# Kernel optimization log

Hardware: AMD Instinct MI355X
Metric: run time of the kernel (lower is better)

The kernel has to match this reference:

```python
import jax, jax.numpy as jnp
import numpy as np

N_NODES = 100000
N_EDGES = 3200000


def _gcn_layer(x, W, b, src, dst, n):
    # DGL GraphConv, norm='both': D_out^{-1/2} A^T D_in^{-1/2} style normalization.
    ones = jnp.ones((src.shape[0],), dtype=x.dtype)
    deg_out = jnp.clip(jax.ops.segment_sum(ones, src, num_segments=n), 1.0)  # out-degree of src
    deg_in = jnp.clip(jax.ops.segment_sum(ones, dst, num_segments=n), 1.0)   # in-degree of dst
    # pre-normalize and project first (in_feats >= out_feats => cheaper messages)
    h = (x * jax.lax.rsqrt(deg_out)[:, None]) @ W            # [N, out]
    agg = jax.ops.segment_sum(h[src], dst, num_segments=n)   # gather + scatter-add over edges
    return agg * jax.lax.rsqrt(deg_in)[:, None] + b


def setup_inputs() -> dict:
    key = jax.random.key(0)
    k1, k2, k3, k4, k5 = jax.random.split(key, 5)
    in_f, h_f, n_cls = 256, 128, 40
    x = jax.random.normal(k1, (N_NODES, in_f), dtype=jnp.float32)
    W1 = jax.random.normal(k2, (in_f, h_f), dtype=jnp.float32) * (1.0 / np.sqrt(in_f))
    b1 = jnp.zeros((h_f,), dtype=jnp.float32)
    W2 = jax.random.normal(k3, (h_f, n_cls), dtype=jnp.float32) * (1.0 / np.sqrt(h_f))
    b2 = jnp.zeros((n_cls,), dtype=jnp.float32)
    src = jax.random.randint(k4, (N_EDGES,), 0, N_NODES, dtype=jnp.int32)
    dst = jax.random.randint(k5, (N_EDGES,), 0, N_NODES, dtype=jnp.int32)
    return {"x": x, "W1": W1, "b1": b1, "W2": W2, "b2": b2, "src": src, "dst": dst}


def reference(x, W1, b1, W2, b2, src, dst):
    n = x.shape[0]
    h = _gcn_layer(x, W1, b1, src, dst, n)
    h = jax.nn.relu(h)
    return _gcn_layer(h, W2, b2, src, dst, n)  # [N, num_classes] logits
```

## Files before the change

### kernel.cpp

```cpp
#include <hip/hip_runtime.h>

#define IN_F 256
#define HID  128
#define NCLS 40
#define NBKT 256
#define BKTSH 9
#define CH 16384
#define CAP 18432

typedef __attribute__((ext_vector_type(8))) short bf16x8;
typedef __attribute__((ext_vector_type(4))) float f32x4;

static __device__ __forceinline__ unsigned short f2bf(float f) {
    unsigned u = __builtin_bit_cast(unsigned, f);
    u += 0x7fffu + ((u >> 16) & 1u);
    return (unsigned short)(u >> 16);
}
static __device__ __forceinline__ float bf2f(unsigned short b) {
    return __builtin_bit_cast(float, ((unsigned)b) << 16);
}

__global__ void initcur_kernel(int* __restrict__ curD, int* __restrict__ curS) {
    int t = threadIdx.x;
    curD[t] = t * CAP;
    curS[t] = t * CAP;
}

__global__ __launch_bounds__(256) void binBoth_kernel(
    const int* __restrict__ src, const int* __restrict__ dst,
    int* __restrict__ curD, int* __restrict__ curS,
    int* __restrict__ bin, unsigned short* __restrict__ bin2, int E) {
    __shared__ int cntD[NBKT], ofsD[NBKT];
    __shared__ int cntS[NBKT], ofsS[NBKT];
    const int tx = threadIdx.x;
    const int be = blockIdx.x * CH;
    const int ee = min(be + CH, E);
    cntD[tx] = 0; cntS[tx] = 0;
    __syncthreads();
    for (int i = be + tx; i < ee; i += 256) {
        atomicAdd(&cntD[dst[i] >> BKTSH], 1);
        atomicAdd(&cntS[src[i] >> BKTSH], 1);
    }
    __syncthreads();
    int c = cntD[tx];
    ofsD[tx] = c ? atomicAdd(&curD[tx], c) : 0;
    cntD[tx] = 0;
    c = cntS[tx];
    ofsS[tx] = c ? atomicAdd(&curS[tx], c) : 0;
    cntS[tx] = 0;
    __syncthreads();
    for (int i = be + tx; i < ee; i += 256) {
        int d = dst[i], s = src[i];
        int b = d >> BKTSH;
        int l = atomicAdd(&cntD[b], 1);
        bin[ofsD[b] + l] = ((d & 511) << 17) | s;
        int b2 = s >> BKTSH;
        int l2 = atomicAdd(&cntS[b2], 1);
        bin2[ofsS[b2] + l2] = (unsigned short)(s & 511);
    }
}

__global__ __launch_bounds__(256) void passB_kernel(
    const int* __restrict__ curD_final, const int* __restrict__ bin,
    int* __restrict__ csr_src, int* __restrict__ row_ptr, int* __restrict__ row_end,
    float* __restrict__ rs_in, int N) {
    __shared__ int cnt[512];
    __shared__ int cur[512];
    __shared__ int part[256];
    const int b = blockIdx.x;
    const int base = b * CAP, end = curD_final[b];
    const int tx = threadIdx.x;
    cnt[tx] = 0; cnt[tx + 256] = 0;
    __syncthreads();
    for (int i = base + tx; i < end; i += 256)
        atomicAdd(&cnt[bin[i] >> 17], 1);
    __syncthreads();
    int a0 = cnt[2 * tx], a1 = cnt[2 * tx + 1];
    part[tx] = a0 + a1;
    __syncthreads();
    for (int off = 1; off < 256; off <<= 1) {
        int v = (tx >= off) ? part[tx - off] : 0;
        __syncthreads();
        part[tx] += v;
        __syncthreads();
    }
    int excl = part[tx] - (a0 + a1);
    cur[2 * tx] = excl;
    cur[2 * tx + 1] = excl + a0;
    int idx = (b << BKTSH) + 2 * tx;
    row_ptr[idx]     = base + excl;
    row_end[idx]     = base + excl + a0;
    row_ptr[idx + 1] = base + excl + a0;
    row_end[idx + 1] = base + excl + a0 + a1;
    if (idx < N)     rs_in[idx]     = rsqrtf((float)max(a0, 1));
    if (idx + 1 < N) rs_in[idx + 1] = rsqrtf((float)max(a1, 1));
    __syncthreads();
    for (int i = base + tx; i < end; i += 256) {
        int v = bin[i];
        int nl = v >> 17;
        int p = atomicAdd(&cur[nl], 1);
        csr_src[base + p] = v & 0x1FFFF;
    }
}

__global__ __launch_bounds__(256) void passBs_kernel(
    const int* __restrict__ curS_final, const unsigned short* __restrict__ bin2,
    float* __restrict__ rs_out, int N) {
    __shared__ int cnt[512];
    const int b = blockIdx.x;
    const int base = b * CAP, end = curS_final[b];
    const int tx = threadIdx.x;
    cnt[tx] = 0; cnt[tx + 256] = 0;
    __syncthreads();
    for (int i = base + tx; i < end; i += 256)
        atomicAdd(&cnt[bin2[i]], 1);
    __syncthreads();
    int idx = (b << BKTSH) + tx;
    if (idx < N)       rs_out[idx]       = rsqrtf((float)max(cnt[tx], 1));
    if (idx + 256 < N) rs_out[idx + 256] = rsqrtf((float)max(cnt[tx + 256], 1));
}

__global__ __launch_bounds__(256) void gemm1_kernel(
    const float* __restrict__ x, const float* __restrict__ W1,
    const float* __restrict__ rs_out, unsigned short* __restrict__ h1b, int N) {
    __shared__ unsigned short Wl[32768];

    const int tx = threadIdx.x;
#pragma unroll
    for (int e = 0; e < 32; ++e) {
        int base = (tx + 256 * e) * 4;
        float4 w = *(const float4*)&W1[base];
        int k = base >> 7;
        int c0 = base & 127;
        float wv[4] = {w.x, w.y, w.z, w.w};
#pragma unroll
        for (int q = 0; q < 4; ++q) {
            int col = c0 + q;
            int byte = col * 512 + k * 2;
            byte ^= (col & 7) << 4;
            Wl[byte >> 1] = f2bf(wv[q]);
        }
    }
    __syncthreads();

    const int wv_ = tx >> 6, lane = tx & 63;
    const int r0 = blockIdx.x * 64 + wv_ * 16;
    const int arow = r0 + (lane & 15);
    const int arow_c = min(arow, N - 1);
    const float rs = rs_out[arow_c];
    const long xbase = (long)arow_c * IN_F + (lane >> 4) * 8;

    bf16x8 a8[8];
#pragma unroll
    for (int ks = 0; ks < 8; ++ks) {
        float4 p0 = *(const float4*)&x[xbase + ks * 32];
        float4 p1 = *(const float4*)&x[xbase + ks * 32 + 4];
        bf16x8 a;
        a[0] = (short)f2bf(p0.x * rs); a[1] = (short)f2bf(p0.y * rs);
        a[2] = (short)f2bf(p0.z * rs); a[3] = (short)f2bf(p0.w * rs);
        a[4] = (short)f2bf(p1.x * rs); a[5] = (short)f2bf(p1.y * rs);
        a[6] = (short)f2bf(p1.z * rs); a[7] = (short)f2bf(p1.w * rs);
        a8[ks] = a;
    }

    f32x4 acc[8];
#pragma unroll
    for (int nf = 0; nf < 8; ++nf) acc[nf] = (f32x4){0.f, 0.f, 0.f, 0.f};

#pragma unroll
    for (int ks = 0; ks < 8; ++ks) {
#pragma unroll
        for (int nf = 0; nf < 8; ++nf) {
            int col = nf * 16 + (lane & 15);
            int kb  = ks * 32 + (lane >> 4) * 8;
            int byte = col * 512 + kb * 2;
            byte ^= (col & 7) << 4;
            bf16x8 b = *(const bf16x8*)((const char*)Wl + byte);
            acc[nf] = __builtin_amdgcn_mfma_f32_16x16x32_bf16(a8[ks], b, acc[nf], 0, 0, 0);
        }
    }

#pragma unroll
    for (int nf = 0; nf < 8; ++nf) {
#pragma unroll
        for (int j = 0; j < 4; ++j) {
            int row = r0 + (lane >> 4) * 4 + j;
            if (row < N)
                h1b[(long)row * HID + nf * 16 + (lane & 15)] = f2bf(acc[nf][j]);
        }
    }
}

__global__ __launch_bounds__(256) void agg1_kernel(
    const int* __restrict__ row_ptr, const int* __restrict__ row_end,
    const int* __restrict__ csr_src, const unsigned* __restrict__ h1b2,
    unsigned* __restrict__ aggb, int N) {
    int node = (blockIdx.x * 256 + threadIdx.x) >> 6;
    int lane = threadIdx.x & 63;
    if (node >= N) return;
    int e = row_ptr[node], end = row_end[node];
    float ax = 0.f, ay = 0.f;
    for (; e + 8 <= end; e += 8) {
        int s0 = csr_src[e],     s1 = csr_src[e + 1], s2 = csr_src[e + 2], s3 = csr_src[e + 3];
        int s4 = csr_src[e + 4], s5 = csr_src[e + 5], s6 = csr_src[e + 6], s7 = csr_src[e + 7];
        unsigned u0 = h1b2[(long)s0 * 64 + lane];
        unsigned u1 = h1b2[(long)s1 * 64 + lane];
        unsigned u2 = h1b2[(long)s2 * 64 + lane];
        unsigned u3 = h1b2[(long)s3 * 64 + lane];
        unsigned u4 = h1b2[(long)s4 * 64 + lane];
        unsigned u5 = h1b2[(long)s5 * 64 + lane];
        unsigned u6 = h1b2[(long)s6 * 64 + lane];
        unsigned u7 = h1b2[(long)s7 * 64 + lane];
        ax += (__builtin_bit_cast(float, u0 << 16) + __builtin_bit_cast(float, u1 << 16))
            + (__builtin_bit_cast(float, u2 << 16) + __builtin_bit_cast(float, u3 << 16))
            + (__builtin_bit_cast(float, u4 << 16) + __builtin_bit_cast(float, u5 << 16))
            + (__builtin_bit_cast(float, u6 << 16) + __builtin_bit_cast(float, u7 << 16));
        ay += (__builtin_bit_cast(float, u0 & 0xffff0000u) + __builtin_bit_cast(float, u1 & 0xffff0000u))
            + (__builtin_bit_cast(float, u2 & 0xffff0000u) + __builtin_bit_cast(float, u3 & 0xffff0000u))
            + (__builtin_bit_cast(float, u4 & 0xffff0000u) + __builtin_bit_cast(float, u5 & 0xffff0000u))
            + (__builtin_bit_cast(float, u6 & 0xffff0000u) + __builtin_bit_cast(float, u7 & 0xffff0000u));
    }
    for (; e < end; ++e) {
        unsigned u = h1b2[(long)csr_src[e] * 64 + lane];
        ax += __builtin_bit_cast(float, u << 16);
        ay += __builtin_bit_cast(float, u & 0xffff0000u);
    }
    aggb[(long)node * 64 + lane] = ((unsigned)f2bf(ay) << 16) | (unsigned)f2bf(ax);
}

__global__ __launch_bounds__(256) void gemm2_kernel(
    const unsigned short* __restrict__ aggb, const float* __restrict__ W2,
    const float* __restrict__ b1, const float* __restrict__ rs_in,
    const float* __restrict__ rs_out, unsigned short* __restrict__ h2p, int N) {
    __shared__ unsigned short Wl[48 * 128];

    const int tx = threadIdx.x;
    for (int idx = tx; idx < 48 * 128; idx += 256) Wl[idx] = 0;
    __syncthreads();
    for (int idx = tx; idx < 128 * NCLS; idx += 256) {
        int k = idx / NCLS, c = idx - k * NCLS;
        int byte = c * 256 + k * 2;
        byte ^= (c & 7) << 4;
        Wl[byte >> 1] = f2bf(W2[idx]);
    }
    __syncthreads();

    const int wv_ = tx >> 6, lane = tx & 63;
    const int r0 = blockIdx.x * 64 + wv_ * 16;
    const int arow = r0 + (lane & 15);
    const int arow_c = min(arow, N - 1);
    const float ri = rs_in[arow_c];
    const float ro = rs_out[arow_c];
    const int k0 = (lane >> 4) * 8;
    const long abase = (long)arow_c * HID + k0;

    bf16x8 a8[4];
#pragma unroll
    for (int ks = 0; ks < 4; ++ks) {
        bf16x8 ar = *(const bf16x8*)&aggb[abase + ks * 32];
        float4 c0 = *(const float4*)&b1[k0 + ks * 32];
        float4 c1 = *(const float4*)&b1[k0 + ks * 32 + 4];
        float bv[8] = {c0.x, c0.y, c0.z, c0.w, c1.x, c1.y, c1.z, c1.w};
        bf16x8 a;
#pragma unroll
        for (int j = 0; j < 8; ++j)
            a[j] = (short)f2bf(fmaxf(fmaf(bf2f((unsigned short)ar[j]), ri, bv[j]), 0.f) * ro);
        a8[ks] = a;
    }

    f32x4 acc[3];
#pragma unroll
    for (int nf = 0; nf < 3; ++nf) acc[nf] = (f32x4){0.f, 0.f, 0.f, 0.f};

#pragma unroll
    for (int ks = 0; ks < 4; ++ks) {
#pragma unroll
        for (int nf = 0; nf < 3; ++nf) {
            int col = nf * 16 + (lane & 15);
            int kb  = ks * 32 + k0;
            int byte = col * 256 + kb * 2;
            byte ^= (col & 7) << 4;
            bf16x8 b = *(const bf16x8*)((const char*)Wl + byte);
            acc[nf] = __builtin_amdgcn_mfma_f32_16x16x32_bf16(a8[ks], b, acc[nf], 0, 0, 0);
        }
    }

#pragma unroll
    for (int nf = 0; nf < 3; ++nf) {
        int col = nf * 16 + (lane & 15);
        if (col < NCLS) {
#pragma unroll
            for (int j = 0; j < 4; ++j) {
                int row = r0 + (lane >> 4) * 4 + j;
                if (row < N)
                    h2p[(long)row * 64 + col] = f2bf(acc[nf][j]);
            }
        }
    }
}

__global__ __launch_bounds__(256) void agg2_kernel(
    const int* __restrict__ row_ptr, const int* __restrict__ row_end,
    const int* __restrict__ csr_src, const unsigned* __restrict__ h2p2,
    const float* __restrict__ rs_in, const float* __restrict__ b2,
    float* __restrict__ out, int N) {
    int i = blockIdx.x * 256 + threadIdx.x;
    if (i >= N * 20) return;
    int node = i / 20;
    int cp   = i - node * 20;
    int e = row_ptr[node], end = row_end[node];
    float ax = 0.f, ay = 0.f;
    for (; e + 4 <= end; e += 4) {
        int s0 = csr_src[e], s1 = csr_src[e + 1], s2 = csr_src[e + 2], s3 = csr_src[e + 3];
        unsigned u0 = h2p2[(long)s0 * 32 + cp];
        unsigned u1 = h2p2[(long)s1 * 32 + cp];
        unsigned u2 = h2p2[(long)s2 * 32 + cp];
        unsigned u3 = h2p2[(long)s3 * 32 + cp];
        ax += __builtin_bit_cast(float, u0 << 16) + __builtin_bit_cast(float, u1 << 16)
            + __builtin_bit_cast(float, u2 << 16) + __builtin_bit_cast(float, u3 << 16);
        ay += __builtin_bit_cast(float, u0 & 0xffff0000u) + __builtin_bit_cast(float, u1 & 0xffff0000u)
            + __builtin_bit_cast(float, u2 & 0xffff0000u) + __builtin_bit_cast(float, u3 & 0xffff0000u);
    }
    for (; e < end; ++e) {
        unsigned u = h2p2[(long)csr_src[e] * 32 + cp];
        ax += __builtin_bit_cast(float, u << 16);
        ay += __builtin_bit_cast(float, u & 0xffff0000u);
    }
    float r = rs_in[node];
    float2 o;
    o.x = fmaf(ax, r, b2[2 * cp]);
    o.y = fmaf(ay, r, b2[2 * cp + 1]);
    *(float2*)&out[(long)node * NCLS + 2 * cp] = o;
}

extern "C" void kernel_launch(void* const* d_in, const int* in_sizes, int n_in,
                              void* d_out, int out_size, void* d_ws, size_t ws_size,
                              hipStream_t stream) {
    const float* x  = (const float*)d_in[0];
    const float* W1 = (const float*)d_in[1];
    const float* b1 = (const float*)d_in[2];
    const float* W2 = (const float*)d_in[3];
    const float* b2 = (const float*)d_in[4];
    const int*  src = (const int*)d_in[5];
    const int*  dst = (const int*)d_in[6];
    const int N = in_sizes[0] / IN_F;
    const int E = in_sizes[5];
    const int NBLK = (N + 511) >> BKTSH;

    float* wsf       = (float*)d_ws;
    float* rs_out    = wsf;
    float* rs_in     = wsf + N;
    int*   curD      = (int*)(wsf + 2 * (long)N);
    int*   curS      = curD + NBKT;
    int*   row_ptr   = curS + NBKT;
    int*   row_end   = row_ptr + N + 1024;
    int*   bin       = row_end + N + 1024;
    int*   csr_src   = bin + (long)NBLK * CAP;
    unsigned short* bin2 = (unsigned short*)(csr_src + (long)NBLK * CAP);
    unsigned short* h1b  = bin2 + (long)NBLK * CAP;
    unsigned short* aggb = h1b + (long)N * HID;
    unsigned short* h2p  = aggb + (long)N * HID;

    initcur_kernel<<<1, 256, 0, stream>>>(curD, curS);
    binBoth_kernel<<<(E + CH - 1) / CH, 256, 0, stream>>>(src, dst, curD, curS,
                                                          bin, bin2, E);
    passB_kernel<<<NBLK, 256, 0, stream>>>(curD, bin, csr_src, row_ptr, row_end, rs_in, N);
    passBs_kernel<<<NBLK, 256, 0, stream>>>(curS, bin2, rs_out, N);

    gemm1_kernel<<<(N + 63) / 64, 256, 0, stream>>>(x, W1, rs_out, h1b, N);
    agg1_kernel<<<(N * 64 + 255) / 256, 256, 0, stream>>>(row_ptr, row_end, csr_src,
                                                          (const unsigned*)h1b,
                                                          (unsigned*)aggb, N);
    gemm2_kernel<<<(N + 63) / 64, 256, 0, stream>>>(aggb, W2, b1, rs_in, rs_out, h2p, N);
    agg2_kernel<<<(N * 20 + 255) / 256, 256, 0, stream>>>(row_ptr, row_end, csr_src,
                                                          (const unsigned*)h2p, rs_in, b2,
                                                          (float*)d_out, N);
}
```

Baseline: 387.5 us.

## Stage edge chunks in LDS, double gemm1 rows per block, unroll agg2 gather

The binning kernel now copies its src/dst chunk into shared memory so the second pass reads LDS instead of re-reading global memory, and the chunk size is halved to make the buffers fit. gemm1 now processes two 64-row tiles per block, so the LDS-staged bf16 conversion of W1 is amortized over twice as many rows. agg2 unrolls its edge gather from 4 to 8 loads in flight and uses a tree-shaped sum. The costs are 64KB of LDS per binning block, which lowers occupancy and doubles the atomics on the global cursors, and half as many gemm1 blocks.

```diff
diff --git a/kernel.cpp b/kernel.cpp
--- a/kernel.cpp
+++ b/kernel.cpp
@@ -5,7 +5,7 @@
 #define NCLS 40
 #define NBKT 256
 #define BKTSH 9
-#define CH 16384
+#define CH 8192
 #define CAP 18432
 
 typedef __attribute__((ext_vector_type(8))) short bf16x8;
@@ -30,16 +30,20 @@
     const int* __restrict__ src, const int* __restrict__ dst,
     int* __restrict__ curD, int* __restrict__ curS,
     int* __restrict__ bin, unsigned short* __restrict__ bin2, int E) {
+    __shared__ int sS[CH];
+    __shared__ int sD[CH];
     __shared__ int cntD[NBKT], ofsD[NBKT];
     __shared__ int cntS[NBKT], ofsS[NBKT];
     const int tx = threadIdx.x;
     const int be = blockIdx.x * CH;
-    const int ee = min(be + CH, E);
+    const int n  = min(CH, E - be);
     cntD[tx] = 0; cntS[tx] = 0;
     __syncthreads();
-    for (int i = be + tx; i < ee; i += 256) {
-        atomicAdd(&cntD[dst[i] >> BKTSH], 1);
-        atomicAdd(&cntS[src[i] >> BKTSH], 1);
+    for (int i = tx; i < n; i += 256) {
+        int d = dst[be + i], s = src[be + i];
+        sD[i] = d; sS[i] = s;
+        atomicAdd(&cntD[d >> BKTSH], 1);
+        atomicAdd(&cntS[s >> BKTSH], 1);
     }
     __syncthreads();
     int c = cntD[tx];
@@ -49,8 +53,8 @@
     ofsS[tx] = c ? atomicAdd(&curS[tx], c) : 0;
     cntS[tx] = 0;
     __syncthreads();
-    for (int i = be + tx; i < ee; i += 256) {
-        int d = dst[i], s = src[i];
+    for (int i = tx; i < n; i += 256) {
+        int d = sD[i], s = sS[i];
         int b = d >> BKTSH;
         int l = atomicAdd(&cntD[b], 1);
         bin[ofsD[b] + l] = ((d & 511) << 17) | s;
@@ -144,49 +148,52 @@
     __syncthreads();
 
     const int wv_ = tx >> 6, lane = tx & 63;
-    const int r0 = blockIdx.x * 64 + wv_ * 16;
-    const int arow = r0 + (lane & 15);
-    const int arow_c = min(arow, N - 1);
-    const float rs = rs_out[arow_c];
-    const long xbase = (long)arow_c * IN_F + (lane >> 4) * 8;
-
-    bf16x8 a8[8];
-#pragma unroll
-    for (int ks = 0; ks < 8; ++ks) {
-        float4 p0 = *(const float4*)&x[xbase + ks * 32];
-        float4 p1 = *(const float4*)&x[xbase + ks * 32 + 4];
-        bf16x8 a;
-        a[0] = (short)f2bf(p0.x * rs); a[1] = (short)f2bf(p0.y * rs);
-        a[2] = (short)f2bf(p0.z * rs); a[3] = (short)f2bf(p0.w * rs);
-        a[4] = (short)f2bf(p1.x * rs); a[5] = (short)f2bf(p1.y * rs);
-        a[6] = (short)f2bf(p1.z * rs); a[7] = (short)f2bf(p1.w * rs);
-        a8[ks] = a;
-    }
-
-    f32x4 acc[8];
-#pragma unroll
-    for (int nf = 0; nf < 8; ++nf) acc[nf] = (f32x4){0.f, 0.f, 0.f, 0.f};
-
-#pragma unroll
-    for (int ks = 0; ks < 8; ++ks) {
+
+    for (int t = 0; t < 2; ++t) {
+        const int r0 = blockIdx.x * 128 + t * 64 + wv_ * 16;
+        const int arow = r0 + (lane & 15);
+        const int arow_c = min(arow, N - 1);
+        const float rs = rs_out[arow_c];
+        const long xbase = (long)arow_c * IN_F + (lane >> 4) * 8;
+
+        bf16x8 a8[8];
+#pragma unroll
+        for (int ks = 0; ks < 8; ++ks) {
+            float4 p0 = *(const float4*)&x[xbase + ks * 32];
+            float4 p1 = *(const float4*)&x[xbase + ks * 32 + 4];
+            bf16x8 a;
+            a[0] = (short)f2bf(p0.x * rs); a[1] = (short)f2bf(p0.y * rs);
+            a[2] = (short)f2bf(p0.z * rs); a[3] = (short)f2bf(p0.w * rs);
+            a[4] = (short)f2bf(p1.x * rs); a[5] = (short)f2bf(p1.y * rs);
+            a[6] = (short)f2bf(p1.z * rs); a[7] = (short)f2bf(p1.w * rs);
+            a8[ks] = a;
+        }
+
+        f32x4 acc[8];
+#pragma unroll
+        for (int nf = 0; nf < 8; ++nf) acc[nf] = (f32x4){0.f, 0.f, 0.f, 0.f};
+
+#pragma unroll
+        for (int ks = 0; ks < 8; ++ks) {
+#pragma unroll
+            for (int nf = 0; nf < 8; ++nf) {
+                int col = nf * 16 + (lane & 15);
+                int kb  = ks * 32 + (lane >> 4) * 8;
+                int byte = col * 512 + kb * 2;
+                byte ^= (col & 7) << 4;
+                bf16x8 b = *(const bf16x8*)((const char*)Wl + byte);
+                acc[nf] = __builtin_amdgcn_mfma_f32_16x16x32_bf16(a8[ks], b, acc[nf], 0, 0, 0);
+            }
+        }
+
 #pragma unroll
         for (int nf = 0; nf < 8; ++nf) {
-            int col = nf * 16 + (lane & 15);
-            int kb  = ks * 32 + (lane >> 4) * 8;
-            int byte = col * 512 + kb * 2;
-            byte ^= (col & 7) << 4;
-            bf16x8 b = *(const bf16x8*)((const char*)Wl + byte);
-            acc[nf] = __builtin_amdgcn_mfma_f32_16x16x32_bf16(a8[ks], b, acc[nf], 0, 0, 0);
-        }
-    }
-
-#pragma unroll
-    for (int nf = 0; nf < 8; ++nf) {
-#pragma unroll
-        for (int j = 0; j < 4; ++j) {
-            int row = r0 + (lane >> 4) * 4 + j;
-            if (row < N)
-                h1b[(long)row * HID + nf * 16 + (lane & 15)] = f2bf(acc[nf][j]);
+#pragma unroll
+            for (int j = 0; j < 4; ++j) {
+                int row = r0 + (lane >> 4) * 4 + j;
+                if (row < N)
+                    h1b[(long)row * HID + nf * 16 + (lane & 15)] = f2bf(acc[nf][j]);
+            }
         }
     }
 }
@@ -310,16 +317,25 @@
     int cp   = i - node * 20;
     int e = row_ptr[node], end = row_end[node];
     float ax = 0.f, ay = 0.f;
-    for (; e + 4 <= end; e += 4) {
-        int s0 = csr_src[e], s1 = csr_src[e + 1], s2 = csr_src[e + 2], s3 = csr_src[e + 3];
+    for (; e + 8 <= end; e += 8) {
+        int s0 = csr_src[e],     s1 = csr_src[e + 1], s2 = csr_src[e + 2], s3 = csr_src[e + 3];
+        int s4 = csr_src[e + 4], s5 = csr_src[e + 5], s6 = csr_src[e + 6], s7 = csr_src[e + 7];
         unsigned u0 = h2p2[(long)s0 * 32 + cp];
         unsigned u1 = h2p2[(long)s1 * 32 + cp];
         unsigned u2 = h2p2[(long)s2 * 32 + cp];
         unsigned u3 = h2p2[(long)s3 * 32 + cp];
-        ax += __builtin_bit_cast(float, u0 << 16) + __builtin_bit_cast(float, u1 << 16)
-            + __builtin_bit_cast(float, u2 << 16) + __builtin_bit_cast(float, u3 << 16);
-        ay += __builtin_bit_cast(float, u0 & 0xffff0000u) + __builtin_bit_cast(float, u1 & 0xffff0000u)
-            + __builtin_bit_cast(float, u2 & 0xffff0000u) + __builtin_bit_cast(float, u3 & 0xffff0000u);
+        unsigned u4 = h2p2[(long)s4 * 32 + cp];
+        unsigned u5 = h2p2[(long)s5 * 32 + cp];
+        unsigned u6 = h2p2[(long)s6 * 32 + cp];
+        unsigned u7 = h2p2[(long)s7 * 32 + cp];
+        ax += (__builtin_bit_cast(float, u0 << 16) + __builtin_bit_cast(float, u1 << 16))
+            + (__builtin_bit_cast(float, u2 << 16) + __builtin_bit_cast(float, u3 << 16))
+            + (__builtin_bit_cast(float, u4 << 16) + __builtin_bit_cast(float, u5 << 16))
+            + (__builtin_bit_cast(float, u6 << 16) + __builtin_bit_cast(float, u7 << 16));
+        ay += (__builtin_bit_cast(float, u0 & 0xffff0000u) + __builtin_bit_cast(float, u1 & 0xffff0000u))
+            + (__builtin_bit_cast(float, u2 & 0xffff0000u) + __builtin_bit_cast(float, u3 & 0xffff0000u))
+            + (__builtin_bit_cast(float, u4 & 0xffff0000u) + __builtin_bit_cast(float, u5 & 0xffff0000u))
+            + (__builtin_bit_cast(float, u6 & 0xffff0000u) + __builtin_bit_cast(float, u7 & 0xffff0000u));
     }
     for (; e < end; ++e) {
         unsigned u = h2p2[(long)csr_src[e] * 32 + cp];
@@ -367,7 +383,7 @@
     passB_kernel<<<NBLK, 256, 0, stream>>>(curD, bin, csr_src, row_ptr, row_end, rs_in, N);
     passBs_kernel<<<NBLK, 256, 0, stream>>>(curS, bin2, rs_out, N);
 
-    gemm1_kernel<<<(N + 63) / 64, 256, 0, stream>>>(x, W1, rs_out, h1b, N);
+    gemm1_kernel<<<(N + 127) / 128, 256, 0, stream>>>(x, W1, rs_out, h1b, N);
     agg1_kernel<<<(N * 64 + 255) / 256, 256, 0, stream>>>(row_ptr, row_end, csr_src,
                                                           (const unsigned*)h1b,
                                                           (unsigned*)aggb, N);
```

New measurement: 356.9 us. 1.09x faster.
